# Kernel tuning notes

Hardware: AMD Instinct MI355X
Metric: run time of the kernel (lower is better)

Reference implementation:

```python
import jax, jax.numpy as jnp
import numpy as np

SEQ_LEN = 2048
BATCH = 64
INPUT_SIZE = 512
HIDDEN_SIZE = 512


def setup_inputs() -> dict:
    key = jax.random.key(0)
    k_x, k_wih, k_whh, k_bih, k_bhh = jax.random.split(key, 5)
    # PyTorch RNN init: U(-1/sqrt(hidden), 1/sqrt(hidden))
    bound = 1.0 / np.sqrt(HIDDEN_SIZE)
    inputs = jax.random.normal(k_x, (SEQ_LEN, BATCH, INPUT_SIZE), dtype=jnp.float32)
    W_ih = jax.random.uniform(k_wih, (HIDDEN_SIZE, INPUT_SIZE), minval=-bound, maxval=bound, dtype=jnp.float32)
    W_hh = jax.random.uniform(k_whh, (HIDDEN_SIZE, HIDDEN_SIZE), minval=-bound, maxval=bound, dtype=jnp.float32)
    b_ih = jax.random.uniform(k_bih, (HIDDEN_SIZE,), minval=-bound, maxval=bound, dtype=jnp.float32)
    b_hh = jax.random.uniform(k_bhh, (HIDDEN_SIZE,), minval=-bound, maxval=bound, dtype=jnp.float32)
    return {"inputs": inputs, "W_ih": W_ih, "W_hh": W_hh, "b_ih": b_ih, "b_hh": b_hh}


def reference(inputs, W_ih, W_hh, b_ih, b_hh):
    # h_t = tanh(x_t W_ih^T + b_ih + h_{t-1} W_hh^T + b_hh)
    # Precompute the input projection for all timesteps in one big GEMM.
    x_proj = jnp.einsum('sbi,hi->sbh', inputs, W_ih) + b_ih + b_hh  # [S, B, H]
    h0 = jnp.zeros((inputs.shape[1], W_hh.shape[0]), dtype=inputs.dtype)

    def step(h, xp):
        h_new = jnp.tanh(xp + h @ W_hh.T)
        return h_new, h_new

    _, out = jax.lax.scan(step, h0, x_proj)  # out: [S, B, H]
    return out.reshape(-1, W_hh.shape[0])  # [S*B, H]
```

## Files before the change

### kernel.cpp

```cpp
#include <hip/hip_runtime.h>
#include <hip/hip_bf16.h>

#define SEQ   2048
#define NBATCH 64
#define HID   512
#define KDIM  512

typedef float f32x4  __attribute__((ext_vector_type(4)));
typedef short bf16x8 __attribute__((ext_vector_type(8)));

__device__ __forceinline__ unsigned short f2bf(float f) {
  union { float f; unsigned int u; } v; v.f = f;
  unsigned int r = v.u + 0x7FFFu + ((v.u >> 16) & 1u);
  return (unsigned short)(r >> 16);
}

__device__ __forceinline__ f32x4 mfma16(bf16x8 a, bf16x8 b, f32x4 c) {
  return __builtin_amdgcn_mfma_f32_16x16x32_bf16(a, b, c, 0, 0, 0);
}

__global__ void prep_wfrag(const float* __restrict__ W, unsigned short* __restrict__ dst) {
  int tid = blockIdx.x * blockDim.x + threadIdx.x;
  int e   = tid & 7;
  int l   = (tid >> 3) & 63;
  int cfg = (tid >> 9) & 31;
  int kf  = tid >> 14;
  int n = cfg * 16 + (l & 15);
  int k = kf * 32 + (l >> 4) * 8 + e;
  dst[tid] = f2bf(W[n * KDIM + k]);
}

__global__ void prep_bsum(const float* __restrict__ a, const float* __restrict__ b,
                          float* __restrict__ out) {
  int j = threadIdx.x;
  if (j < HID) out[j] = a[j] + b[j];
}

__global__ __launch_bounds__(512) void rnn_xproj(
    const float* __restrict__ X,
    const uint4* __restrict__ BW,
    const float* __restrict__ bsum,
    float* __restrict__ out) {
  const int tid = threadIdx.x, w = tid >> 6, l = tid & 63;
  const int g = l >> 4, lr = l & 15;
  const int rowbase = blockIdx.x * 64 + (w >> 2) * 32;
  const int colw = (w & 3) * 128;

  f32x4 acc[2][8];
  #pragma unroll
  for (int cf = 0; cf < 8; ++cf) {
    float bv = bsum[colw + cf * 16 + lr];
    f32x4 z = {bv, bv, bv, bv};
    acc[0][cf] = z; acc[1][cf] = z;
  }

  #pragma unroll 1
  for (int kc = 0; kc < 16; ++kc) {
    const int kb = kc * 32 + g * 8;
    bf16x8 afr[2];
    #pragma unroll
    for (int ai = 0; ai < 2; ++ai) {
      const float* src = X + (size_t)(rowbase + ai * 16 + lr) * KDIM + kb;
      float4 lo = *reinterpret_cast<const float4*>(src);
      float4 hi = *reinterpret_cast<const float4*>(src + 4);
      bf16x8 a;
      a[0] = (short)f2bf(lo.x); a[1] = (short)f2bf(lo.y);
      a[2] = (short)f2bf(lo.z); a[3] = (short)f2bf(lo.w);
      a[4] = (short)f2bf(hi.x); a[5] = (short)f2bf(hi.y);
      a[6] = (short)f2bf(hi.z); a[7] = (short)f2bf(hi.w);
      afr[ai] = a;
    }
    #pragma unroll
    for (int cf = 0; cf < 8; ++cf) {
      const int cfg = (w & 3) * 8 + cf;
      uint4 braw = BW[(kc * 32 + cfg) * 64 + l];
      bf16x8 b = __builtin_bit_cast(bf16x8, braw);
      acc[0][cf] = mfma16(afr[0], b, acc[0][cf]);
      acc[1][cf] = mfma16(afr[1], b, acc[1][cf]);
    }
  }

  #pragma unroll
  for (int ai = 0; ai < 2; ++ai) {
    #pragma unroll
    for (int cf = 0; cf < 8; ++cf) {
      const int col = colw + cf * 16 + lr;
      #pragma unroll
      for (int r = 0; r < 4; ++r) {
        const int row = rowbase + ai * 16 + g * 4 + r;
        out[(size_t)row * HID + col] = acc[ai][cf][r];
      }
    }
  }
}

__global__ __launch_bounds__(512, 2) void rnn_scan(
    const uint4* __restrict__ BW,
    float* __restrict__ xo) {
  extern __shared__ char smem[];
  const int tid = threadIdx.x, w = tid >> 6, l = tid & 63;
  const int g = l >> 4, lr = l & 15;
  const int bg = blockIdx.x;

  {
    uint4* lb = reinterpret_cast<uint4*>(smem);
    #pragma unroll
    for (int i = 0; i < 16; ++i) lb[i * 512 + tid] = BW[i * 512 + tid];
  }
  {
    float* hz = reinterpret_cast<float*>(smem + 147456);
    #pragma unroll
    for (int i = 0; i < 8; ++i) hz[i * 512 + tid] = 0.f;
  }
  bf16x8 ar[12][4];
  #pragma unroll
  for (int kf = 0; kf < 12; ++kf)
    #pragma unroll
    for (int mf = 0; mf < 4; ++mf)
      ar[kf][mf] = __builtin_bit_cast(bf16x8,
          BW[((kf + 4) * 32 + (w * 4 + mf)) * 64 + l]);
  __syncthreads();

  const int hoff = l * 16;
  const int apre = (w * 4) * 1024 + l * 16;
  const int hwb  = (w * 2) * 1024 + (g >> 1) * 256 + (g & 1) * 8 + lr * 16;
  float* xrow0 = xo + ((size_t)bg * 16 + lr) * HID + (size_t)(w * 4) * 16 + g * 4;

#define HB(kf, RD) (*reinterpret_cast<const bf16x8*>(                            \
    smem + 131072 + (RD) + (kf) * 1024 + hoff))
#define AF(kf, mf) (*reinterpret_cast<const bf16x8*>(                            \
    smem + (kf) * 32768 + apre + (mf) * 1024))

  f32x4 xv[4];
  #pragma unroll
  for (int mf = 0; mf < 4; ++mf)
    xv[mf] = *reinterpret_cast<const f32x4*>(xrow0 + mf * 16);
  bf16x8 pa0 = AF(0, 0), pa1 = AF(0, 1), pa2 = AF(0, 2), pa3 = AF(0, 3);

#define SCAN_STEP(S, RD, WR)                                                      \
  {                                                                               \
    const int s = (S);                                                            \
    f32x4 acc[4];                                                                 \
    _Pragma("unroll")                                                             \
    for (int mf = 0; mf < 4; ++mf) acc[mf] = xv[mf];                              \
    {          \
      const float* xn = xrow0 + (size_t)(s + 1 < SEQ ? s + 1 : s) * (64 * HID);   \
      _Pragma("unroll")                                                           \
      for (int mf = 0; mf < 4; ++mf)                                              \
        xv[mf] = *reinterpret_cast<const f32x4*>(xn + mf * 16);                   \
    }                                                                             \
              \
    {                                                                             \
      bf16x8 hb = HB(0, RD);                                                      \
      acc[0] = mfma16(pa0, hb, acc[0]);                                           \
      acc[1] = mfma16(pa1, hb, acc[1]);                                           \
      acc[2] = mfma16(pa2, hb, acc[2]);                                           \
      acc[3] = mfma16(pa3, hb, acc[3]);                                           \
    }                                                                             \
                                                                \
    _Pragma("unroll")                                                             \
    for (int kf = 1; kf < 4; ++kf) {                                              \
      bf16x8 hb = HB(kf, RD);                                                     \
      const char* ab = smem + kf * 32768 + apre;                                  \
      acc[0] = mfma16(*reinterpret_cast<const bf16x8*>(ab       ), hb, acc[0]);   \
      acc[1] = mfma16(*reinterpret_cast<const bf16x8*>(ab + 1024), hb, acc[1]);   \
      acc[2] = mfma16(*reinterpret_cast<const bf16x8*>(ab + 2048), hb, acc[2]);   \
      acc[3] = mfma16(*reinterpret_cast<const bf16x8*>(ab + 3072), hb, acc[3]);   \
    }                                                                             \
                                                               \
    _Pragma("unroll")                                                             \
    for (int kf = 0; kf < 12; ++kf) {                                             \
      bf16x8 hb = HB(kf + 4, RD);                                                 \
      acc[0] = mfma16(ar[kf][0], hb, acc[0]);                                     \
      acc[1] = mfma16(ar[kf][1], hb, acc[1]);                                     \
      acc[2] = mfma16(ar[kf][2], hb, acc[2]);                                     \
      acc[3] = mfma16(ar[kf][3], hb, acc[3]);                                     \
    }                                                                             \
          \
    float* orow = xrow0 + (size_t)s * (64 * HID);                                 \
    _Pragma("unroll")                                                             \
    for (int mf = 0; mf < 4; ++mf) {                                              \
      f32x4 hv;                                                                   \
      _Pragma("unroll")                                                           \
      for (int r = 0; r < 4; ++r) {                                               \
        const float pre = acc[mf][r];                                             \
        hv[r] = 1.0f - 2.0f * __builtin_amdgcn_rcpf(1.0f + __expf(2.0f * pre));   \
      }                                                                           \
      *reinterpret_cast<f32x4*>(orow + mf * 16) = hv;                             \
      uint2 hp;                                                                   \
      hp.x = (unsigned)f2bf(hv[0]) | ((unsigned)f2bf(hv[1]) << 16);               \
      hp.y = (unsigned)f2bf(hv[2]) | ((unsigned)f2bf(hv[3]) << 16);               \
      *reinterpret_cast<uint2*>(smem + 131072 + (WR) + hwb +                      \
          (mf >> 1) * 1024 + (mf & 1) * 512) = hp;                                \
    }                                                                             \
       \
                        \
    pa0 = AF(0, 0); pa1 = AF(0, 1); pa2 = AF(0, 2); pa3 = AF(0, 3);               \
    asm volatile("s_waitcnt lgkmcnt(0)\n\ts_barrier" ::: "memory");               \
  }

  #pragma unroll 1
  for (int s2 = 0; s2 < SEQ; s2 += 2) {
    SCAN_STEP(s2,     16384, 0)
    SCAN_STEP(s2 + 1, 0,     16384)
  }
#undef SCAN_STEP
#undef HB
#undef AF
}

extern "C" void kernel_launch(void* const* d_in, const int* in_sizes, int n_in,
                              void* d_out, int out_size, void* d_ws, size_t ws_size,
                              hipStream_t stream) {
  (void)in_sizes; (void)n_in; (void)out_size;
  const float* X   = (const float*)d_in[0];
  const float* Wih = (const float*)d_in[1];
  const float* Whh = (const float*)d_in[2];
  const float* bih = (const float*)d_in[3];
  const float* bhh = (const float*)d_in[4];
  float* out = (float*)d_out;

  unsigned short* wihf = (unsigned short*)d_ws;
  unsigned short* whhf = wihf + 262144;
  float* bsum = (float*)(whhf + 262144);
  if (ws_size < (size_t)(2 * 524288 + 2048)) return;

  prep_wfrag<<<1024, 256, 0, stream>>>(Wih, wihf);
  prep_wfrag<<<1024, 256, 0, stream>>>(Whh, whhf);
  prep_bsum<<<1, 512, 0, stream>>>(bih, bhh, bsum);

  rnn_xproj<<<2048, 512, 0, stream>>>(X, (const uint4*)wihf, bsum, out);

  hipFuncSetAttribute(reinterpret_cast<const void*>(rnn_scan),
                      hipFuncAttributeMaxDynamicSharedMemorySize, 163840);
  rnn_scan<<<4, 512, 163840, stream>>>((const uint4*)whhf, out);
}
```

Measured before the change: 5.028 ms.

## Restructure RNN scan step: deeper A-fragment prefetch, late x load, packed bf16 convert

Each recurrence step now prefetches two k-fragments of LDS-resident weights (eight registers) across the barrier instead of one. It also loads the x-projection for the current step mid-loop instead of one step ahead, and uses v_cvt_pk_bf16_f32 in place of the manual bf16 rounding. The barrier now waits with lgkmcnt(8) rather than 0, so the weight prefetch reads stay in flight across it. The aim is to shorten the serial critical path per timestep, at the cost of extra register pressure and a barrier wait count that must track the exact number of outstanding LDS operations.

New measurement: 4.912 ms. -2.3%, faster.

```diff
diff --git a/kernel.cpp b/kernel.cpp
--- a/kernel.cpp
+++ b/kernel.cpp
@@ -131,72 +131,82 @@
 #define AF(kf, mf) (*reinterpret_cast<const bf16x8*>(                            \
     smem + (kf) * 32768 + apre + (mf) * 1024))
 
-  f32x4 xv[4];
-  #pragma unroll
-  for (int mf = 0; mf < 4; ++mf)
-    xv[mf] = *reinterpret_cast<const f32x4*>(xrow0 + mf * 16);
   bf16x8 pa0 = AF(0, 0), pa1 = AF(0, 1), pa2 = AF(0, 2), pa3 = AF(0, 3);
+  bf16x8 pa4 = AF(1, 0), pa5 = AF(1, 1), pa6 = AF(1, 2), pa7 = AF(1, 3);
 
 #define SCAN_STEP(S, RD, WR)                                                      \
   {                                                                               \
     const int s = (S);                                                            \
-    f32x4 acc[4];                                                                 \
-    _Pragma("unroll")                                                             \
-    for (int mf = 0; mf < 4; ++mf) acc[mf] = xv[mf];                              \
-    {          \
-      const float* xn = xrow0 + (size_t)(s + 1 < SEQ ? s + 1 : s) * (64 * HID);   \
-      _Pragma("unroll")                                                           \
-      for (int mf = 0; mf < 4; ++mf)                                              \
-        xv[mf] = *reinterpret_cast<const f32x4*>(xn + mf * 16);                   \
-    }                                                                             \
-              \
+    f32x4 acc0 = {0,0,0,0}, acc1 = {0,0,0,0}, acc2 = {0,0,0,0}, acc3 = {0,0,0,0}; \
+                         \
     {                                                                             \
       bf16x8 hb = HB(0, RD);                                                      \
-      acc[0] = mfma16(pa0, hb, acc[0]);                                           \
-      acc[1] = mfma16(pa1, hb, acc[1]);                                           \
-      acc[2] = mfma16(pa2, hb, acc[2]);                                           \
-      acc[3] = mfma16(pa3, hb, acc[3]);                                           \
-    }                                                                             \
-                                                                \
+      acc0 = mfma16(pa0, hb, acc0); acc1 = mfma16(pa1, hb, acc1);                 \
+      acc2 = mfma16(pa2, hb, acc2); acc3 = mfma16(pa3, hb, acc3);                 \
+    }                                                                             \
+    {                                                                             \
+      bf16x8 hb = HB(1, RD);                                                      \
+      acc0 = mfma16(pa4, hb, acc0); acc1 = mfma16(pa5, hb, acc1);                 \
+      acc2 = mfma16(pa6, hb, acc2); acc3 = mfma16(pa7, hb, acc3);                 \
+    }                                                                             \
+                                                           \
     _Pragma("unroll")                                                             \
-    for (int kf = 1; kf < 4; ++kf) {                                              \
+    for (int kf = 2; kf < 4; ++kf) {                                              \
       bf16x8 hb = HB(kf, RD);                                                     \
       const char* ab = smem + kf * 32768 + apre;                                  \
-      acc[0] = mfma16(*reinterpret_cast<const bf16x8*>(ab       ), hb, acc[0]);   \
-      acc[1] = mfma16(*reinterpret_cast<const bf16x8*>(ab + 1024), hb, acc[1]);   \
-      acc[2] = mfma16(*reinterpret_cast<const bf16x8*>(ab + 2048), hb, acc[2]);   \
-      acc[3] = mfma16(*reinterpret_cast<const bf16x8*>(ab + 3072), hb, acc[3]);   \
-    }                                                                             \
+      acc0 = mfma16(*reinterpret_cast<const bf16x8*>(ab       ), hb, acc0);       \
+      acc1 = mfma16(*reinterpret_cast<const bf16x8*>(ab + 1024), hb, acc1);       \
+      acc2 = mfma16(*reinterpret_cast<const bf16x8*>(ab + 2048), hb, acc2);       \
+      acc3 = mfma16(*reinterpret_cast<const bf16x8*>(ab + 3072), hb, acc3);       \
+    }                                                                             \
+                      \
+    const float* xrs = xrow0 + (size_t)s * (64 * HID);                            \
+    f32x4 xt0 = *reinterpret_cast<const f32x4*>(xrs);                             \
+    f32x4 xt1 = *reinterpret_cast<const f32x4*>(xrs + 16);                        \
+    f32x4 xt2 = *reinterpret_cast<const f32x4*>(xrs + 32);                        \
+    f32x4 xt3 = *reinterpret_cast<const f32x4*>(xrs + 48);                        \
                                                                \
     _Pragma("unroll")                                                             \
     for (int kf = 0; kf < 12; ++kf) {                                             \
       bf16x8 hb = HB(kf + 4, RD);                                                 \
-      acc[0] = mfma16(ar[kf][0], hb, acc[0]);                                     \
-      acc[1] = mfma16(ar[kf][1], hb, acc[1]);                                     \
-      acc[2] = mfma16(ar[kf][2], hb, acc[2]);                                     \
-      acc[3] = mfma16(ar[kf][3], hb, acc[3]);                                     \
-    }                                                                             \
-          \
+      acc0 = mfma16(ar[kf][0], hb, acc0);                                         \
+      acc1 = mfma16(ar[kf][1], hb, acc1);                                         \
+      acc2 = mfma16(ar[kf][2], hb, acc2);                                         \
+      acc3 = mfma16(ar[kf][3], hb, acc3);                                         \
+    }                                                                             \
+                      \
     float* orow = xrow0 + (size_t)s * (64 * HID);                                 \
+    f32x4 hv0, hv1, hv2, hv3;                                                     \
     _Pragma("unroll")                                                             \
-    for (int mf = 0; mf < 4; ++mf) {                                              \
-      f32x4 hv;                                                                   \
-      _Pragma("unroll")                                                           \
-      for (int r = 0; r < 4; ++r) {                                               \
-        const float pre = acc[mf][r];                                             \
-        hv[r] = 1.0f - 2.0f * __builtin_amdgcn_rcpf(1.0f + __expf(2.0f * pre));   \
-      }                                                                           \
-      *reinterpret_cast<f32x4*>(orow + mf * 16) = hv;                             \
-      uint2 hp;                                                                   \
-      hp.x = (unsigned)f2bf(hv[0]) | ((unsigned)f2bf(hv[1]) << 16);               \
-      hp.y = (unsigned)f2bf(hv[2]) | ((unsigned)f2bf(hv[3]) << 16);               \
-      *reinterpret_cast<uint2*>(smem + 131072 + (WR) + hwb +                      \
-          (mf >> 1) * 1024 + (mf & 1) * 512) = hp;                                \
-    }                                                                             \
+    for (int r = 0; r < 4; ++r) {                                                 \
+      hv0[r] = 1.0f - 2.0f * __builtin_amdgcn_rcpf(1.0f + __expf(2.0f * (acc0[r] + xt0[r]))); \
+      hv1[r] = 1.0f - 2.0f * __builtin_amdgcn_rcpf(1.0f + __expf(2.0f * (acc1[r] + xt1[r]))); \
+      hv2[r] = 1.0f - 2.0f * __builtin_amdgcn_rcpf(1.0f + __expf(2.0f * (acc2[r] + xt2[r]))); \
+      hv3[r] = 1.0f - 2.0f * __builtin_amdgcn_rcpf(1.0f + __expf(2.0f * (acc3[r] + xt3[r]))); \
+    }                                                                             \
+    *reinterpret_cast<f32x4*>(orow)      = hv0;                                   \
+    *reinterpret_cast<f32x4*>(orow + 16) = hv1;                                   \
+    *reinterpret_cast<f32x4*>(orow + 32) = hv2;                                   \
+    *reinterpret_cast<f32x4*>(orow + 48) = hv3;                                   \
+    uint2 hp;                                                                     \
+    asm("v_cvt_pk_bf16_f32 %0, %1, %2" : "=v"(hp.x) : "v"(hv0[0]), "v"(hv0[1])); \
+    asm("v_cvt_pk_bf16_f32 %0, %1, %2" : "=v"(hp.y) : "v"(hv0[2]), "v"(hv0[3])); \
+    *reinterpret_cast<uint2*>(smem + 131072 + (WR) + hwb)        = hp;            \
+    asm("v_cvt_pk_bf16_f32 %0, %1, %2" : "=v"(hp.x) : "v"(hv1[0]), "v"(hv1[1])); \
+    asm("v_cvt_pk_bf16_f32 %0, %1, %2" : "=v"(hp.y) : "v"(hv1[2]), "v"(hv1[3])); \
+    *reinterpret_cast<uint2*>(smem + 131072 + (WR) + hwb + 512)  = hp;            \
+    asm("v_cvt_pk_bf16_f32 %0, %1, %2" : "=v"(hp.x) : "v"(hv2[0]), "v"(hv2[1])); \
+    asm("v_cvt_pk_bf16_f32 %0, %1, %2" : "=v"(hp.y) : "v"(hv2[2]), "v"(hv2[3])); \
+    *reinterpret_cast<uint2*>(smem + 131072 + (WR) + hwb + 1024) = hp;            \
+    asm("v_cvt_pk_bf16_f32 %0, %1, %2" : "=v"(hp.x) : "v"(hv3[0]), "v"(hv3[1])); \
+    asm("v_cvt_pk_bf16_f32 %0, %1, %2" : "=v"(hp.y) : "v"(hv3[2]), "v"(hv3[3])); \
+    *reinterpret_cast<uint2*>(smem + 131072 + (WR) + hwb + 1536) = hp;            \
+        \
+    __builtin_amdgcn_sched_barrier(0);                                            \
+    pa0 = AF(0, 0); pa1 = AF(0, 1); pa2 = AF(0, 2); pa3 = AF(0, 3);               \
+    pa4 = AF(1, 0); pa5 = AF(1, 1); pa6 = AF(1, 2); pa7 = AF(1, 3);               \
        \
-                        \
-    pa0 = AF(0, 0); pa1 = AF(0, 1); pa2 = AF(0, 2); pa3 = AF(0, 3);               \
-    asm volatile("s_waitcnt lgkmcnt(0)\n\ts_barrier" ::: "memory");               \
+    asm volatile("s_waitcnt lgkmcnt(8)\n\ts_barrier" ::: "memory");               \
   }
 
   #pragma unroll 1
```
